# Kernel optimization log

Measured on AMD Instinct MI355X. Metric: run time of the kernel, lower is better.

The kernel has to match this reference:

```python
import jax, jax.numpy as jnp
import numpy as np

N, E, R, K1, F = 50000, 400000, 1000, 1000, 128
DEPTH, HEADS = 1, 2

def _l2norm(x, axis):
    n = jnp.sqrt(jnp.maximum(jnp.sum(x * x, axis=axis, keepdims=True), 1e-12))
    return x / n

def _segment_softmax(logits, seg, num_segments):
    m = jax.ops.segment_max(logits, seg, num_segments=num_segments)
    e = jnp.exp(logits - m[seg])
    s = jax.ops.segment_sum(e, seg, num_segments=num_segments)
    return e / s[seg]

def setup_inputs() -> dict:
    rng = np.random.RandomState(0)
    # adjacency: nodes 0..K1-1 have exactly one edge (long-tail), rest random rows
    rows = np.concatenate([np.arange(K1), rng.randint(K1, N, size=E - K1)])
    cols = rng.randint(0, N, size=E)
    order = np.lexsort((cols, rows))
    adj = np.stack([rows, cols], axis=1)[order].astype(np.int32)  # [E,2] sorted by row
    self_nodes_idx = np.arange(K1, dtype=np.int32)
    neights_node_idxs = adj[:K1, 1].astype(np.int32)  # neighbor of each degree-1 node
    sparse_indices = np.stack([np.arange(E), rng.randint(0, R, size=E)], axis=1).astype(np.int32)
    sparse_val = (rng.rand(E).astype(np.float32) * 0.5 + 0.5)
    key = jax.random.key(0)
    k = jax.random.split(key, 5)
    return {
        'features': jax.random.normal(k[0], (N, F), jnp.float32),
        'rel_emb': jax.random.normal(k[1], (R, F), jnp.float32),
        'sparse_val': jnp.asarray(sparse_val),
        'attn_kernels': jax.random.normal(k[2], (DEPTH, HEADS, F), jnp.float32) * (1.0 / np.sqrt(F)),
        'proxy': jax.random.normal(k[3], (64, F * (DEPTH + 1)), jnp.float32) * 0.1,
        'gate_kernel': jax.random.normal(k[4], (F * (DEPTH + 1), F * (DEPTH + 1)), jnp.float32) * (1.0 / np.sqrt(F * (DEPTH + 1))),
        'adj_indices': jnp.asarray(adj),
        'sparse_indices': jnp.asarray(sparse_indices),
        'self_nodes_idx': jnp.asarray(self_nodes_idx),
        'neights_node_idxs': jnp.asarray(neights_node_idxs),
    }

def reference(features, rel_emb, sparse_val, attn_kernels, proxy, gate_kernel,
              adj_indices, sparse_indices, self_nodes_idx, neights_node_idxs):
    row = adj_indices[:, 0]
    col = adj_indices[:, 1]
    feats = features  # activation is linear (None)
    outputs = [feats]
    for l in range(DEPTH):
        # per-triple relation embedding: sparse (E,R) @ rel_emb -> (E,F)
        rels_sum = jax.ops.segment_sum(sparse_val[:, None] * rel_emb[sparse_indices[:, 1]],
                                       sparse_indices[:, 0], num_segments=E)
        rels_norm = _l2norm(rels_sum, axis=1)  # l2 normalize rows
        neighs = feats[col]  # [E,F] gather
        # Householder reflection of neighbor features by relation direction
        neighs = neighs - 2.0 * jnp.sum(neighs * rels_norm, axis=1, keepdims=True) * rels_norm
        head_feats = []
        for head in range(HEADS):
            att_logits = rels_sum @ attn_kernels[l, head]  # [E]
            att = _segment_softmax(att_logits, row, N)  # sparse softmax per destination node
            nf = jax.ops.segment_sum(neighs * att[:, None], row, num_segments=N)  # [N,F]
            if head == 1:
                # long-tail fix: degree-1 nodes copy their single neighbor's aggregated feature
                nf = nf.at[self_nodes_idx].set(nf[neights_node_idxs])
            head_feats.append(nf)
        feats = jnp.mean(jnp.stack(head_feats, axis=0), axis=0)
        outputs.append(feats)
    out = jnp.concatenate(outputs, axis=-1)  # [N, F*(DEPTH+1)]
    proxy_att = jax.nn.softmax(_l2norm(out, axis=-1) @ _l2norm(proxy, axis=-1).T, axis=-1)  # [N,64]
    proxy_feature = out - proxy_att @ proxy
    gate = jax.nn.sigmoid(proxy_feature @ gate_kernel)
    return gate * out + (1.0 - gate) * proxy_feature
```

## Files before the change

### kernel.cpp

```cpp
#include <hip/hip_runtime.h>
#include <math.h>

constexpr int N  = 50000;
constexpr int E  = 400000;
constexpr int R  = 1000;
constexpr int K1 = 1000;
constexpr int F  = 128;
constexpr int OUTC = 256;
constexpr int P  = 64;

typedef _Float16 f16x8 __attribute__((ext_vector_type(8)));
typedef _Float16 f16x4 __attribute__((ext_vector_type(4)));
typedef _Float16 f16x2 __attribute__((ext_vector_type(2)));
typedef float f32x4 __attribute__((ext_vector_type(4)));

#if __has_builtin(__builtin_amdgcn_fdot2)
#define FDOT2(a, b, c) __builtin_amdgcn_fdot2((a), (b), (c), false)
#else
#define FDOT2(a, b, c) fmaf((float)(a)[0], (float)(b)[0], fmaf((float)(a)[1], (float)(b)[1], (c)))
#endif

__device__ inline float waveReduceSum(float v) {
#pragma unroll
    for (int m = 32; m >= 1; m >>= 1) v += __shfl_xor(v, m, 64);
    return v;
}

constexpr int B_FEATSH = 3125;
constexpr int B_REL    = 250;
constexpr int B_SEG    = 1563;
constexpr int B_PSC    = 16;
constexpr int B_PGF    = 64;

__global__ __launch_bounds__(256) void prep_a(
        const float* __restrict__ feats, const float* __restrict__ rel_emb,
        const float* __restrict__ attn,  const float* __restrict__ proxy,
        const float* __restrict__ G,     const int* __restrict__ adj,
        _Float16* __restrict__ featsH,   _Float16* __restrict__ relnormH,
        float* __restrict__ dotr, int* __restrict__ nstart, int* __restrict__ nend,
        float* __restrict__ pscale, float* __restrict__ PGf) {
    int b = blockIdx.x, tid = threadIdx.x;
    if (b < B_FEATSH) {
        int idx = b * 256 + tid;
        float4 x0 = ((const float4*)feats)[2 * idx];
        float4 x1 = ((const float4*)feats)[2 * idx + 1];
        f16x8 h;
        h[0] = (_Float16)x0.x; h[1] = (_Float16)x0.y;
        h[2] = (_Float16)x0.z; h[3] = (_Float16)x0.w;
        h[4] = (_Float16)x1.x; h[5] = (_Float16)x1.y;
        h[6] = (_Float16)x1.z; h[7] = (_Float16)x1.w;
        ((f16x8*)featsH)[idx] = h;
    } else if (b < B_FEATSH + B_REL) {
        int r = (b - B_FEATSH) * 4 + (tid >> 6);
        int lane = tid & 63;
        float2 v  = ((const float2*)(rel_emb + (size_t)r * F))[lane];
        float2 a0 = ((const float2*)attn)[lane];
        float2 a1 = ((const float2*)attn)[64 + lane];
        float ss = waveReduceSum(v.x * v.x + v.y * v.y);
        float d0 = waveReduceSum(v.x * a0.x + v.y * a0.y);
        float d1 = waveReduceSum(v.x * a1.x + v.y * a1.y);
        float sc = rsqrtf(fmaxf(ss, 1e-12f));
        f16x2 h; h[0] = (_Float16)(v.x * sc); h[1] = (_Float16)(v.y * sc);
        ((f16x2*)(relnormH + (size_t)r * F))[lane] = h;
        if (lane == 0) { dotr[2 * r] = d0; dotr[2 * r + 1] = d1; }
    } else if (b < B_FEATSH + B_REL + B_SEG) {
        int e = (b - B_FEATSH - B_REL) * 256 + tid;
        if (e < E) {
            int lane = tid & 63;
            int row = ((const int2*)adj)[e].x;
            int prev = __shfl_up(row, 1, 64);
            if (lane == 0) prev = (e > 0) ? ((const int2*)adj)[e - 1].x : -1;
            int nxt = __shfl_down(row, 1, 64);
            if (lane == 63 && e + 1 < E) nxt = ((const int2*)adj)[e + 1].x;
            if (prev != row) {
                nstart[row] = e;
                for (int rr = prev + 1; rr < row; ++rr) { nstart[rr] = e; nend[rr] = e; }
            }
            if (e == E - 1) {
                nend[row] = E;
                for (int rr = row + 1; rr < N; ++rr) { nstart[rr] = E; nend[rr] = E; }
            } else if (nxt != row) {
                nend[row] = e + 1;
            }
        }
    } else if (b < B_FEATSH + B_REL + B_SEG + B_PSC) {
        int j = (b - B_FEATSH - B_REL - B_SEG) * 4 + (tid >> 6);
        int lane = tid & 63;
        float4 p = ((const float4*)(proxy + (size_t)j * OUTC))[lane];
        float ss = waveReduceSum(p.x * p.x + p.y * p.y + p.z * p.z + p.w * p.w);
        if (lane == 0) pscale[j] = rsqrtf(fmaxf(ss, 1e-12f));
    } else {
        int p = b - (B_FEATSH + B_REL + B_SEG + B_PSC);
        int c = tid;
        float s = 0.f;
        for (int k = 0; k < OUTC; ++k)
            s = fmaf(proxy[(size_t)p * OUTC + k], G[(size_t)k * OUTC + c], s);
        PGf[(size_t)p * OUTC + c] = s;
    }
}

constexpr int NB_NODE = N / 4;
constexpr int NB_FRAG = 56;

__global__ __launch_bounds__(256) void node_frag(
        const _Float16* __restrict__ featsH,
        const _Float16* __restrict__ relnormH,
        const float* __restrict__ dotr,
        const int* __restrict__ adj,
        const int* __restrict__ sidx,
        const float* __restrict__ val,
        const int* __restrict__ nstart,
        const int* __restrict__ nend,
        const float* __restrict__ G,
        const float* __restrict__ proxy,
        const float* __restrict__ pscale,
        const float* __restrict__ PGf,
        _Float16* __restrict__ nf0,
        _Float16* __restrict__ nf1,
        f16x8* __restrict__ Gh, f16x8* __restrict__ pnH,
        f16x8* __restrict__ pxH, f16x8* __restrict__ pgH) {
    if (blockIdx.x >= NB_NODE) {
        int u = (blockIdx.x - NB_NODE) * 4 + (threadIdx.x >> 6);
        int L = threadIdx.x & 63;
        int q = L >> 4, m = L & 15;
        f16x8 h;
        if (u < 128) {
            int kk = u >> 4, cg = u & 15;
            int n = cg * 16 + m;
#pragma unroll
            for (int j = 0; j < 8; ++j)
                h[j] = (_Float16)G[(size_t)(kk * 32 + q * 8 + j) * OUTC + n];
            Gh[(size_t)u * 64 + L] = h;
        } else if (u < 160) {
            int idx = u - 128;
            int kk = idx >> 2, w = idx & 3;
            int n = w * 16 + m;
            float sc = pscale[n];
#pragma unroll
            for (int j = 0; j < 8; ++j)
                h[j] = (_Float16)(proxy[(size_t)n * OUTC + kk * 32 + q * 8 + j] * sc);
            pnH[(size_t)idx * 64 + L] = h;
        } else if (u < 192) {
            int idx = u - 160;
            int kk = idx >> 4, cg = idx & 15;
            int n = cg * 16 + m;
#pragma unroll
            for (int j = 0; j < 8; ++j)
                h[j] = (_Float16)proxy[(size_t)(kk * 32 + q * 8 + j) * OUTC + n];
            pxH[(size_t)idx * 64 + L] = h;
        } else {
            int idx = u - 192;
            int kk = idx >> 4, cg = idx & 15;
            int n = cg * 16 + m;
#pragma unroll
            for (int j = 0; j < 8; ++j)
                h[j] = (_Float16)(-PGf[(size_t)(kk * 32 + q * 8 + j) * OUTC + n]);
            pgH[(size_t)idx * 64 + L] = h;
        }
        return;
    }
    int n = blockIdx.x * 4 + (threadIdx.x >> 6);
    int lane = threadIdx.x & 63;
    int g = lane >> 4, gl = lane & 15;
    int start = nstart[n], end = nend[n];
    const int2* adj2 = (const int2*)adj;
    const int2* sx2  = (const int2*)sidx;
    float A0[8], A1[8];
#pragma unroll
    for (int j = 0; j < 8; ++j) { A0[j] = 0.f; A1[j] = 0.f; }
    float s0 = 0.f, s1 = 0.f;
    for (int e = start + g; e < end; e += 8) {
        int eB = e + 4;
        bool hasB = (eB < end);
        int eBc = hasB ? eB : e;
        int colA = adj2[e].y,   colB = adj2[eBc].y;
        int relA = sx2[e].y,    relB = sx2[eBc].y;
        float vA = val[e],      vB = val[eBc];
        float2 drA = ((const float2*)dotr)[relA];
        float2 drB = ((const float2*)dotr)[relB];
        float wA0 = __expf(vA * drA.x), wA1 = __expf(vA * drA.y);
        float wB0 = hasB ? __expf(vB * drB.x) : 0.f;
        float wB1 = hasB ? __expf(vB * drB.y) : 0.f;
        s0 += wA0 + wB0; s1 += wA1 + wB1;
        f16x8 fAv = ((const f16x8*)(featsH   + (size_t)colA * F))[gl];
        f16x8 rAv = ((const f16x8*)(relnormH + (size_t)relA * F))[gl];
        f16x8 fBv = ((const f16x8*)(featsH   + (size_t)colB * F))[gl];
        f16x8 rBv = ((const f16x8*)(relnormH + (size_t)relB * F))[gl];
        const f16x2* fA2 = (const f16x2*)&fAv;
        const f16x2* rA2 = (const f16x2*)&rAv;
        const f16x2* fB2 = (const f16x2*)&fBv;
        const f16x2* rB2 = (const f16x2*)&rBv;
        float pdA = 0.f, pdB = 0.f;
#pragma unroll
        for (int j = 0; j < 4; ++j) {
            pdA = FDOT2(fA2[j], rA2[j], pdA);
            pdB = FDOT2(fB2[j], rB2[j], pdB);
        }
        pdA += __shfl_xor(pdA, 1, 64); pdB += __shfl_xor(pdB, 1, 64);
        pdA += __shfl_xor(pdA, 2, 64); pdB += __shfl_xor(pdB, 2, 64);
        pdA += __shfl_xor(pdA, 4, 64); pdB += __shfl_xor(pdB, 4, 64);
        pdA += __shfl_xor(pdA, 8, 64); pdB += __shfl_xor(pdB, 8, 64);
        _Float16 tAh = (_Float16)(2.f * pdA), tBh = (_Float16)(2.f * pdB);
        f16x2 tA2; tA2[0] = tAh; tA2[1] = tAh;
        f16x2 tB2; tB2[0] = tBh; tB2[1] = tBh;
#pragma unroll
        for (int j = 0; j < 4; ++j) {
            f16x2 rxA = fA2[j] - tA2 * rA2[j];
            f16x2 rxB = fB2[j] - tB2 * rB2[j];
            float x0 = (float)rxA[0], x1 = (float)rxA[1];
            float y0 = (float)rxB[0], y1 = (float)rxB[1];
            A0[2*j]   = fmaf(wA0, x0, A0[2*j]);   A0[2*j]   = fmaf(wB0, y0, A0[2*j]);
            A0[2*j+1] = fmaf(wA0, x1, A0[2*j+1]); A0[2*j+1] = fmaf(wB0, y1, A0[2*j+1]);
            A1[2*j]   = fmaf(wA1, x0, A1[2*j]);   A1[2*j]   = fmaf(wB1, y0, A1[2*j]);
            A1[2*j+1] = fmaf(wA1, x1, A1[2*j+1]); A1[2*j+1] = fmaf(wB1, y1, A1[2*j+1]);
        }
    }
#pragma unroll
    for (int j = 0; j < 8; ++j) {
        A0[j] += __shfl_xor(A0[j], 16, 64); A0[j] += __shfl_xor(A0[j], 32, 64);
        A1[j] += __shfl_xor(A1[j], 16, 64); A1[j] += __shfl_xor(A1[j], 32, 64);
    }
    s0 += __shfl_xor(s0, 16, 64); s0 += __shfl_xor(s0, 32, 64);
    s1 += __shfl_xor(s1, 16, 64); s1 += __shfl_xor(s1, 32, 64);
    float i0 = (s0 > 0.f) ? 1.f / s0 : 0.f;
    float i1 = (s1 > 0.f) ? 1.f / s1 : 0.f;
    if (g == 0) {
        f16x8 h0, h1;
#pragma unroll
        for (int j = 0; j < 8; ++j) {
            h0[j] = (_Float16)(A0[j] * i0);
            h1[j] = (_Float16)(A1[j] * i1);
        }
        ((f16x8*)(nf0 + (size_t)n * F))[gl] = h0;
        ((f16x8*)(nf1 + (size_t)n * F))[gl] = h1;
    }
}

__global__ __launch_bounds__(512, 6) void proxy_gate(
        const _Float16* __restrict__ featsH,
        const _Float16* __restrict__ nf0,
        const _Float16* __restrict__ nf1,
        const int* __restrict__ neigh,
        const f16x8* __restrict__ pnH,
        const f16x8* __restrict__ pxH,
        const f16x8* __restrict__ Gh,
        const f16x8* __restrict__ pgH,
        float* __restrict__ out) {
    constexpr int LDA = 68;
    __shared__ __align__(16) f16x8 outH[16 * 64];
    __shared__ __align__(16) float attL[32 * LDA];
    __shared__ float scaleL[32];
    int tid = threadIdx.x;
    int w = tid >> 6, lane = tid & 63;
    int quad = lane >> 4, m = lane & 15;
    size_t row0 = (size_t)blockIdx.x * 32;

    {
        int bm = tid >> 4, gl = tid & 15;
        int n = (int)row0 + bm;
        float ss;
        f16x8 h1, h2;
        if (n < N) {
            ss = 0.f;
            h1 = ((const f16x8*)(featsH + (size_t)n * F))[gl];
#pragma unroll
            for (int j = 0; j < 8; ++j) { float x = (float)h1[j]; ss += x * x; }
            int sel = (n < K1) ? neigh[n] : n;
            f16x8 a  = ((const f16x8*)(nf0 + (size_t)n   * F))[gl];
            f16x8 b2 = ((const f16x8*)(nf1 + (size_t)sel * F))[gl];
#pragma unroll
            for (int j = 0; j < 8; ++j) {
                float v = 0.5f * ((float)a[j] + (float)b2[j]);
                h2[j] = (_Float16)v;
                ss += v * v;
            }
        } else {
#pragma unroll
            for (int j = 0; j < 8; ++j) { h1[j] = (_Float16)0.f; h2[j] = (_Float16)0.f; }
            ss = 1.f;
        }
        int t = bm >> 4, r16 = bm & 15;
        outH[(t * 8 +     (gl >> 2)) * 64 + (gl & 3) * 16 + r16] = h1;
        outH[(t * 8 + 4 + (gl >> 2)) * 64 + (gl & 3) * 16 + r16] = h2;
        ss += __shfl_xor(ss, 1, 64); ss += __shfl_xor(ss, 2, 64);
        ss += __shfl_xor(ss, 4, 64); ss += __shfl_xor(ss, 8, 64);
        if (gl == 0) scaleL[bm] = rsqrtf(fmaxf(ss, 1e-12f));
    }
    __syncthreads();

    int tl = w >> 2;
    int pg = w & 3;
    f32x4 lacc = (f32x4){0,0,0,0};
    f32x4 zacc[2][2];
#pragma unroll
    for (int t = 0; t < 2; ++t)
#pragma unroll
        for (int c = 0; c < 2; ++c) zacc[t][c] = (f32x4){0,0,0,0};
#pragma unroll
    for (int kk = 0; kk < 8; ++kk) {
        f16x8 pb  = pnH[(size_t)(kk * 4 + pg) * 64 + lane];
        f16x8 gb0 = Gh[(size_t)(kk * 16 + w)     * 64 + lane];
        f16x8 gb1 = Gh[(size_t)(kk * 16 + w + 8) * 64 + lane];
        f16x8 a0 = outH[(0 * 8 + kk) * 64 + lane];
        f16x8 a1 = outH[(1 * 8 + kk) * 64 + lane];
        f16x8 at = tl ? a1 : a0;
        lacc       = __builtin_amdgcn_mfma_f32_16x16x32_f16(at, pb,  lacc,       0, 0, 0);
        zacc[0][0] = __builtin_amdgcn_mfma_f32_16x16x32_f16(a0, gb0, zacc[0][0], 0, 0, 0);
        zacc[0][1] = __builtin_amdgcn_mfma_f32_16x16x32_f16(a0, gb1, zacc[0][1], 0, 0, 0);
        zacc[1][0] = __builtin_amdgcn_mfma_f32_16x16x32_f16(a1, gb0, zacc[1][0], 0, 0, 0);
        zacc[1][1] = __builtin_amdgcn_mfma_f32_16x16x32_f16(a1, gb1, zacc[1][1], 0, 0, 0);
    }
#pragma unroll
    for (int i = 0; i < 4; ++i) {
        int r = tl * 16 + quad * 4 + i;
        attL[r * LDA + pg * 16 + m] = lacc[i] * scaleL[r];
    }
    __syncthreads();

#pragma unroll
    for (int i = 0; i < 4; ++i) {
        int r = 4 * w + i;
        float e = __expf(attL[r * LDA + lane]);
        float s = waveReduceSum(e);
        attL[r * LDA + lane] = e / s;
    }
    __syncthreads();

    f32x4 qacc[2][2];
#pragma unroll
    for (int t = 0; t < 2; ++t)
#pragma unroll
        for (int c = 0; c < 2; ++c) qacc[t][c] = (f32x4){0,0,0,0};
#pragma unroll
    for (int kk = 0; kk < 2; ++kk) {
        f16x8 a[2];
#pragma unroll
        for (int t = 0; t < 2; ++t) {
            const float4* ap = (const float4*)&attL[(t * 16 + m) * LDA + kk * 32 + quad * 8];
            float4 x = ap[0], y = ap[1];
            a[t][0]=(_Float16)x.x; a[t][1]=(_Float16)x.y; a[t][2]=(_Float16)x.z; a[t][3]=(_Float16)x.w;
            a[t][4]=(_Float16)y.x; a[t][5]=(_Float16)y.y; a[t][6]=(_Float16)y.z; a[t][7]=(_Float16)y.w;
        }
#pragma unroll
        for (int cgi = 0; cgi < 2; ++cgi) {
            int cg = w + 8 * cgi;
            f16x8 bx = pxH[(size_t)(kk * 16 + cg) * 64 + lane];
            f16x8 bg = pgH[(size_t)(kk * 16 + cg) * 64 + lane];
#pragma unroll
            for (int t = 0; t < 2; ++t) {
                qacc[t][cgi] = __builtin_amdgcn_mfma_f32_16x16x32_f16(a[t], bx, qacc[t][cgi], 0, 0, 0);
                zacc[t][cgi] = __builtin_amdgcn_mfma_f32_16x16x32_f16(a[t], bg, zacc[t][cgi], 0, 0, 0);
            }
        }
    }

    const _Float16* outHs = (const _Float16*)outH;
#pragma unroll
    for (int t = 0; t < 2; ++t) {
        if ((int)row0 + t * 16 >= N) continue;
#pragma unroll
        for (int cgi = 0; cgi < 2; ++cgi) {
            int cg = w + 8 * cgi;
            int c = cg * 16 + m;
            int kkc = cg >> 1;
            int qc = ((cg & 1) << 1) | (m >> 3);
            int j = m & 7;
#pragma unroll
            for (int i = 0; i < 4; ++i) {
                int r15 = quad * 4 + i;
                float ov = (float)outHs[(((t * 8 + kkc) * 64 + qc * 16 + r15) << 3) + j];
                float gate = 1.f / (1.f + __expf(-zacc[t][cgi][i]));
                size_t n = row0 + t * 16 + r15;
                out[n * OUTC + c] = ov - (1.f - gate) * qacc[t][cgi][i];
            }
        }
    }
}

extern "C" void kernel_launch(void* const* d_in, const int* in_sizes, int n_in,
                              void* d_out, int out_size, void* d_ws, size_t ws_size,
                              hipStream_t stream) {
    const float* features   = (const float*)d_in[0];
    const float* rel_emb    = (const float*)d_in[1];
    const float* sparse_val = (const float*)d_in[2];
    const float* attn       = (const float*)d_in[3];
    const float* proxy      = (const float*)d_in[4];
    const float* gateK      = (const float*)d_in[5];
    const int*   adj        = (const int*)d_in[6];
    const int*   sidx       = (const int*)d_in[7];
    const int*   neigh      = (const int*)d_in[9];
    float* out = (float*)d_out;

    char* ws = (char*)d_ws;
    size_t off = 0;
    auto alloc = [&](size_t bytes) -> void* {
        void* p = ws + off;
        off += (bytes + 255) & ~(size_t)255;
        return p;
    };
    _Float16* relnormH = (_Float16*)alloc((size_t)R * F * 2);
    float*    dotr     = (float*)alloc((size_t)R * 2 * 4);
    float*    pscale   = (float*)alloc((size_t)P * 4);
    float*    PGf      = (float*)alloc((size_t)P * OUTC * 4);
    f16x8*    Gh       = (f16x8*)alloc((size_t)128 * 64 * 16);
    f16x8*    pnH      = (f16x8*)alloc((size_t)32 * 64 * 16);
    f16x8*    pxH      = (f16x8*)alloc((size_t)32 * 64 * 16);
    f16x8*    pgH      = (f16x8*)alloc((size_t)32 * 64 * 16);
    _Float16* featsH   = (_Float16*)alloc((size_t)N * F * 2);
    int*      nstart   = (int*)alloc((size_t)N * 4);
    int*      nend     = (int*)alloc((size_t)N * 4);
    _Float16* nf0      = (_Float16*)alloc((size_t)N * F * 2);
    _Float16* nf1      = (_Float16*)alloc((size_t)N * F * 2);

    prep_a<<<B_FEATSH + B_REL + B_SEG + B_PSC + B_PGF, 256, 0, stream>>>(
        features, rel_emb, attn, proxy, gateK, adj,
        featsH, relnormH, dotr, nstart, nend, pscale, PGf);
    node_frag<<<NB_NODE + NB_FRAG, 256, 0, stream>>>(
        featsH, relnormH, dotr, adj, sidx, sparse_val, nstart, nend,
        gateK, proxy, pscale, PGf,
        nf0, nf1, Gh, pnH, pxH, pgH);
    proxy_gate<<<(N + 31) / 32, 512, 0, stream>>>(
        featsH, nf0, nf1, neigh, pnH, pxH, Gh, pgH, out);
}
```

Baseline: 172.8 us.

## Make proxy_gate persistent and keep weight fragments in registers across tiles

The proxy_gate kernel now launches a fixed grid of 256 blocks that loop over 32-row tiles. Each block loads the proxy, gate and proxy-gate MFMA B fragments into registers once instead of once per tile. Launch bounds drop to 2 blocks per SM to make room for the extra registers, and a trailing barrier guards LDS reuse between iterations. The trade-off is lower occupancy and less latency hiding for the gather loads of nf0, nf1 and featsH, with no overlap added between the load phase and the MFMA phase.

```diff
diff --git a/kernel.cpp b/kernel.cpp
--- a/kernel.cpp
+++ b/kernel.cpp
@@ -236,7 +236,8 @@
     }
 }
 
-__global__ __launch_bounds__(512, 6) void proxy_gate(
+constexpr int PG_GRID = 256;
+__global__ __launch_bounds__(512, 2) void proxy_gate(
         const _Float16* __restrict__ featsH,
         const _Float16* __restrict__ nf0,
         const _Float16* __restrict__ nf1,
@@ -253,127 +254,141 @@
     int tid = threadIdx.x;
     int w = tid >> 6, lane = tid & 63;
     int quad = lane >> 4, m = lane & 15;
-    size_t row0 = (size_t)blockIdx.x * 32;
-
-    {
-        int bm = tid >> 4, gl = tid & 15;
-        int n = (int)row0 + bm;
-        float ss;
-        f16x8 h1, h2;
-        if (n < N) {
-            ss = 0.f;
-            h1 = ((const f16x8*)(featsH + (size_t)n * F))[gl];
-#pragma unroll
-            for (int j = 0; j < 8; ++j) { float x = (float)h1[j]; ss += x * x; }
-            int sel = (n < K1) ? neigh[n] : n;
-            f16x8 a  = ((const f16x8*)(nf0 + (size_t)n   * F))[gl];
-            f16x8 b2 = ((const f16x8*)(nf1 + (size_t)sel * F))[gl];
-#pragma unroll
-            for (int j = 0; j < 8; ++j) {
-                float v = 0.5f * ((float)a[j] + (float)b2[j]);
-                h2[j] = (_Float16)v;
-                ss += v * v;
-            }
-        } else {
-#pragma unroll
-            for (int j = 0; j < 8; ++j) { h1[j] = (_Float16)0.f; h2[j] = (_Float16)0.f; }
-            ss = 1.f;
-        }
-        int t = bm >> 4, r16 = bm & 15;
-        outH[(t * 8 +     (gl >> 2)) * 64 + (gl & 3) * 16 + r16] = h1;
-        outH[(t * 8 + 4 + (gl >> 2)) * 64 + (gl & 3) * 16 + r16] = h2;
-        ss += __shfl_xor(ss, 1, 64); ss += __shfl_xor(ss, 2, 64);
-        ss += __shfl_xor(ss, 4, 64); ss += __shfl_xor(ss, 8, 64);
-        if (gl == 0) scaleL[bm] = rsqrtf(fmaxf(ss, 1e-12f));
-    }
-    __syncthreads();
-
     int tl = w >> 2;
     int pg = w & 3;
-    f32x4 lacc = (f32x4){0,0,0,0};
-    f32x4 zacc[2][2];
-#pragma unroll
-    for (int t = 0; t < 2; ++t)
-#pragma unroll
-        for (int c = 0; c < 2; ++c) zacc[t][c] = (f32x4){0,0,0,0};
+
+    f16x8 pnF[8], ghF[8][2], pxF[2][2], pgF[2][2];
 #pragma unroll
     for (int kk = 0; kk < 8; ++kk) {
-        f16x8 pb  = pnH[(size_t)(kk * 4 + pg) * 64 + lane];
-        f16x8 gb0 = Gh[(size_t)(kk * 16 + w)     * 64 + lane];
-        f16x8 gb1 = Gh[(size_t)(kk * 16 + w + 8) * 64 + lane];
-        f16x8 a0 = outH[(0 * 8 + kk) * 64 + lane];
-        f16x8 a1 = outH[(1 * 8 + kk) * 64 + lane];
-        f16x8 at = tl ? a1 : a0;
-        lacc       = __builtin_amdgcn_mfma_f32_16x16x32_f16(at, pb,  lacc,       0, 0, 0);
-        zacc[0][0] = __builtin_amdgcn_mfma_f32_16x16x32_f16(a0, gb0, zacc[0][0], 0, 0, 0);
-        zacc[0][1] = __builtin_amdgcn_mfma_f32_16x16x32_f16(a0, gb1, zacc[0][1], 0, 0, 0);
-        zacc[1][0] = __builtin_amdgcn_mfma_f32_16x16x32_f16(a1, gb0, zacc[1][0], 0, 0, 0);
-        zacc[1][1] = __builtin_amdgcn_mfma_f32_16x16x32_f16(a1, gb1, zacc[1][1], 0, 0, 0);
-    }
-#pragma unroll
-    for (int i = 0; i < 4; ++i) {
-        int r = tl * 16 + quad * 4 + i;
-        attL[r * LDA + pg * 16 + m] = lacc[i] * scaleL[r];
-    }
-    __syncthreads();
-
-#pragma unroll
-    for (int i = 0; i < 4; ++i) {
-        int r = 4 * w + i;
-        float e = __expf(attL[r * LDA + lane]);
-        float s = waveReduceSum(e);
-        attL[r * LDA + lane] = e / s;
-    }
-    __syncthreads();
-
-    f32x4 qacc[2][2];
-#pragma unroll
-    for (int t = 0; t < 2; ++t)
-#pragma unroll
-        for (int c = 0; c < 2; ++c) qacc[t][c] = (f32x4){0,0,0,0};
-#pragma unroll
-    for (int kk = 0; kk < 2; ++kk) {
-        f16x8 a[2];
+        pnF[kk]    = pnH[(size_t)(kk * 4 + pg) * 64 + lane];
+        ghF[kk][0] = Gh[(size_t)(kk * 16 + w)     * 64 + lane];
+        ghF[kk][1] = Gh[(size_t)(kk * 16 + w + 8) * 64 + lane];
+    }
+#pragma unroll
+    for (int kk = 0; kk < 2; ++kk)
+#pragma unroll
+        for (int c = 0; c < 2; ++c) {
+            pxF[kk][c] = pxH[(size_t)(kk * 16 + w + 8 * c) * 64 + lane];
+            pgF[kk][c] = pgH[(size_t)(kk * 16 + w + 8 * c) * 64 + lane];
+        }
+
+    int bm = tid >> 4, gl = tid & 15;
+    int t_b = bm >> 4, r16 = bm & 15;
+
+    for (int tp = blockIdx.x; tp * 32 < N; tp += PG_GRID) {
+        size_t row0 = (size_t)tp * 32;
+
+        {
+            int n = (int)row0 + bm;
+            float ss;
+            f16x8 h1, h2;
+            if (n < N) {
+                ss = 0.f;
+                h1 = ((const f16x8*)(featsH + (size_t)n * F))[gl];
+#pragma unroll
+                for (int j = 0; j < 8; ++j) { float x = (float)h1[j]; ss += x * x; }
+                int sel = (n < K1) ? neigh[n] : n;
+                f16x8 a  = ((const f16x8*)(nf0 + (size_t)n   * F))[gl];
+                f16x8 b2 = ((const f16x8*)(nf1 + (size_t)sel * F))[gl];
+#pragma unroll
+                for (int j = 0; j < 8; ++j) {
+                    float v = 0.5f * ((float)a[j] + (float)b2[j]);
+                    h2[j] = (_Float16)v;
+                    ss += v * v;
+                }
+            } else {
+#pragma unroll
+                for (int j = 0; j < 8; ++j) { h1[j] = (_Float16)0.f; h2[j] = (_Float16)0.f; }
+                ss = 1.f;
+            }
+            outH[(t_b * 8 +     (gl >> 2)) * 64 + (gl & 3) * 16 + r16] = h1;
+            outH[(t_b * 8 + 4 + (gl >> 2)) * 64 + (gl & 3) * 16 + r16] = h2;
+            ss += __shfl_xor(ss, 1, 64); ss += __shfl_xor(ss, 2, 64);
+            ss += __shfl_xor(ss, 4, 64); ss += __shfl_xor(ss, 8, 64);
+            if (gl == 0) scaleL[bm] = rsqrtf(fmaxf(ss, 1e-12f));
+        }
+        __syncthreads();
+
+        f32x4 lacc = (f32x4){0,0,0,0};
+        f32x4 zacc[2][2];
+#pragma unroll
+        for (int t = 0; t < 2; ++t)
+#pragma unroll
+            for (int c = 0; c < 2; ++c) zacc[t][c] = (f32x4){0,0,0,0};
+#pragma unroll
+        for (int kk = 0; kk < 8; ++kk) {
+            f16x8 a0 = outH[(0 * 8 + kk) * 64 + lane];
+            f16x8 a1 = outH[(1 * 8 + kk) * 64 + lane];
+            f16x8 at = tl ? a1 : a0;
+            lacc       = __builtin_amdgcn_mfma_f32_16x16x32_f16(at, pnF[kk],    lacc,       0, 0, 0);
+            zacc[0][0] = __builtin_amdgcn_mfma_f32_16x16x32_f16(a0, ghF[kk][0], zacc[0][0], 0, 0, 0);
+            zacc[0][1] = __builtin_amdgcn_mfma_f32_16x16x32_f16(a0, ghF[kk][1], zacc[0][1], 0, 0, 0);
+            zacc[1][0] = __builtin_amdgcn_mfma_f32_16x16x32_f16(a1, ghF[kk][0], zacc[1][0], 0, 0, 0);
+            zacc[1][1] = __builtin_amdgcn_mfma_f32_16x16x32_f16(a1, ghF[kk][1], zacc[1][1], 0, 0, 0);
+        }
+#pragma unroll
+        for (int i = 0; i < 4; ++i) {
+            int r = tl * 16 + quad * 4 + i;
+            attL[r * LDA + pg * 16 + m] = lacc[i] * scaleL[r];
+        }
+        __syncthreads();
+
+#pragma unroll
+        for (int i = 0; i < 4; ++i) {
+            int r = 4 * w + i;
+            float e = __expf(attL[r * LDA + lane]);
+            float s = waveReduceSum(e);
+            attL[r * LDA + lane] = e / s;
+        }
+        __syncthreads();
+
+        f32x4 qacc[2][2];
+#pragma unroll
+        for (int t = 0; t < 2; ++t)
+#pragma unroll
+            for (int c = 0; c < 2; ++c) qacc[t][c] = (f32x4){0,0,0,0};
+#pragma unroll
+        for (int kk = 0; kk < 2; ++kk) {
+            f16x8 a[2];
+#pragma unroll
+            for (int t = 0; t < 2; ++t) {
+                const float4* ap = (const float4*)&attL[(t * 16 + m) * LDA + kk * 32 + quad * 8];
+                float4 x = ap[0], y = ap[1];
+                a[t][0]=(_Float16)x.x; a[t][1]=(_Float16)x.y; a[t][2]=(_Float16)x.z; a[t][3]=(_Float16)x.w;
+                a[t][4]=(_Float16)y.x; a[t][5]=(_Float16)y.y; a[t][6]=(_Float16)y.z; a[t][7]=(_Float16)y.w;
+            }
+#pragma unroll
+            for (int cgi = 0; cgi < 2; ++cgi) {
+#pragma unroll
+                for (int t = 0; t < 2; ++t) {
+                    qacc[t][cgi] = __builtin_amdgcn_mfma_f32_16x16x32_f16(a[t], pxF[kk][cgi], qacc[t][cgi], 0, 0, 0);
+                    zacc[t][cgi] = __builtin_amdgcn_mfma_f32_16x16x32_f16(a[t], pgF[kk][cgi], zacc[t][cgi], 0, 0, 0);
+                }
+            }
+        }
+
+        const _Float16* outHs = (const _Float16*)outH;
 #pragma unroll
         for (int t = 0; t < 2; ++t) {
-            const float4* ap = (const float4*)&attL[(t * 16 + m) * LDA + kk * 32 + quad * 8];
-            float4 x = ap[0], y = ap[1];
-            a[t][0]=(_Float16)x.x; a[t][1]=(_Float16)x.y; a[t][2]=(_Float16)x.z; a[t][3]=(_Float16)x.w;
-            a[t][4]=(_Float16)y.x; a[t][5]=(_Float16)y.y; a[t][6]=(_Float16)y.z; a[t][7]=(_Float16)y.w;
-        }
-#pragma unroll
-        for (int cgi = 0; cgi < 2; ++cgi) {
-            int cg = w + 8 * cgi;
-            f16x8 bx = pxH[(size_t)(kk * 16 + cg) * 64 + lane];
-            f16x8 bg = pgH[(size_t)(kk * 16 + cg) * 64 + lane];
-#pragma unroll
-            for (int t = 0; t < 2; ++t) {
-                qacc[t][cgi] = __builtin_amdgcn_mfma_f32_16x16x32_f16(a[t], bx, qacc[t][cgi], 0, 0, 0);
-                zacc[t][cgi] = __builtin_amdgcn_mfma_f32_16x16x32_f16(a[t], bg, zacc[t][cgi], 0, 0, 0);
-            }
-        }
-    }
-
-    const _Float16* outHs = (const _Float16*)outH;
-#pragma unroll
-    for (int t = 0; t < 2; ++t) {
-        if ((int)row0 + t * 16 >= N) continue;
-#pragma unroll
-        for (int cgi = 0; cgi < 2; ++cgi) {
-            int cg = w + 8 * cgi;
-            int c = cg * 16 + m;
-            int kkc = cg >> 1;
-            int qc = ((cg & 1) << 1) | (m >> 3);
-            int j = m & 7;
-#pragma unroll
-            for (int i = 0; i < 4; ++i) {
-                int r15 = quad * 4 + i;
-                float ov = (float)outHs[(((t * 8 + kkc) * 64 + qc * 16 + r15) << 3) + j];
-                float gate = 1.f / (1.f + __expf(-zacc[t][cgi][i]));
-                size_t n = row0 + t * 16 + r15;
-                out[n * OUTC + c] = ov - (1.f - gate) * qacc[t][cgi][i];
-            }
-        }
+            if ((int)row0 + t * 16 >= N) continue;
+#pragma unroll
+            for (int cgi = 0; cgi < 2; ++cgi) {
+                int cg = w + 8 * cgi;
+                int c = cg * 16 + m;
+                int kkc = cg >> 1;
+                int qc = ((cg & 1) << 1) | (m >> 3);
+                int j = m & 7;
+#pragma unroll
+                for (int i = 0; i < 4; ++i) {
+                    int r15 = quad * 4 + i;
+                    float ov = (float)outHs[(((t * 8 + kkc) * 64 + qc * 16 + r15) << 3) + j];
+                    float gate = 1.f / (1.f + __expf(-zacc[t][cgi][i]));
+                    size_t n = row0 + t * 16 + r15;
+                    out[n * OUTC + c] = ov - (1.f - gate) * qacc[t][cgi][i];
+                }
+            }
+        }
+        __syncthreads();
     }
 }
 
@@ -419,6 +434,6 @@
         featsH, relnormH, dotr, adj, sidx, sparse_val, nstart, nend,
         gateK, proxy, pscale, PGf,
         nf0, nf1, Gh, pnH, pxH, pgH);
-    proxy_gate<<<(N + 31) / 32, 512, 0, stream>>>(
+    proxy_gate<<<PG_GRID, 512, 0, stream>>>(
         featsH, nf0, nf1, neigh, pnH, pxH, Gh, pgH, out);
 }
```

Result: slower. 178.4 us (+3.3%).
